# Kernel tuning notes

Hardware: AMD Instinct MI355X
Metric: run time of the kernel (lower is better)

Reference implementation:

```python
import jax, jax.numpy as jnp
import numpy as np

D_EMBED = 64      # per-head dim (module uses d_embed as head dim)
N_HEADS = 8
SCALE = 1.0 / float(np.sqrt(D_EMBED))
ROPE_BASE = 10000.0


def _rope(x):
    # torchtune-style interleaved RoPE. x: [B, S, H, D]
    B, S, H, D = x.shape
    freqs = 1.0 / (ROPE_BASE ** (jnp.arange(0, D, 2, dtype=jnp.float32) / D))  # [D/2]
    ang = jnp.arange(S, dtype=jnp.float32)[:, None] * freqs[None, :]           # [S, D/2]
    cos = jnp.cos(ang)[None, :, None, :]
    sin = jnp.sin(ang)[None, :, None, :]
    x1 = x[..., 0::2]
    x2 = x[..., 1::2]
    return jnp.stack([x1 * cos - x2 * sin, x1 * sin + x2 * cos], axis=-1).reshape(B, S, H, D)


def setup_inputs() -> dict:
    key = jax.random.key(0)
    ks = jax.random.split(key, 5)
    B, S, D, H = 2, 2048, D_EMBED, N_HEADS
    std = 1.0 / np.sqrt(D)
    return {
        "q": jax.random.normal(ks[0], (B, S, D), jnp.float32),
        "Wq": jax.random.normal(ks[1], (H * D, D), jnp.float32) * std,
        "Wk": jax.random.normal(ks[2], (H * D, D), jnp.float32) * std,
        "Wv": jax.random.normal(ks[3], (H * D, D), jnp.float32) * std,
        "Wo": jax.random.normal(ks[4], (D, H * D), jnp.float32) * std,
        "gamma": jnp.ones((H,), jnp.float32),
    }


def reference(q, Wq, Wk, Wv, Wo, gamma):
    B, S, D = q.shape
    H = N_HEADS
    qh = (q @ Wq.T).reshape(B, S, H, D)
    kh = (q @ Wk.T).reshape(B, S, H, D)
    vh = (q @ Wv.T).reshape(B, S, H, D)
    qh = _rope(qh).transpose(0, 2, 1, 3)  # [B,H,S,D]
    kh = _rope(kh).transpose(0, 2, 1, 3)
    vh = vh.transpose(0, 2, 1, 3)
    # RBF attention scores
    qn = jnp.sum(qh * qh, axis=-1, keepdims=True)                 # [B,H,S,1]
    kn = jnp.sum(kh * kh, axis=-1, keepdims=True)                 # [B,H,S,1]
    qk = jnp.einsum('bhsd,bhtd->bhst', qh, kh)                    # [B,H,S,S]
    dist = jnp.maximum(qn - 2.0 * qk + jnp.swapaxes(kn, -2, -1), 0.0)
    scores = jnp.exp(-(gamma[None, :, None, None] * SCALE) * dist)
    causal = jnp.tril(jnp.ones((S, S), dtype=bool))
    scores = jnp.where(causal, scores, 0.0)
    out = jnp.einsum('bhst,bhtd->bhsd', scores, vh)
    out = out.transpose(0, 2, 1, 3).reshape(B, S, H * D)
    return out @ Wo.T
```

## Files before the change

### kernel.cpp

```cpp
#include <hip/hip_runtime.h>
#include <hip/hip_bf16.h>

#define BB 2
#define SS 2048
#define DD 64
#define HH 8
#define HD 512
#define SCALE 0.125f

typedef __bf16 bf16;
typedef __attribute__((ext_vector_type(4))) __bf16 bf16x4;
typedef __attribute__((ext_vector_type(8))) __bf16 bf16x8;
typedef __attribute__((ext_vector_type(4))) float floatx4;

#define PSLOT 2097152

__device__ __forceinline__ floatx4 mfma16(bf16x8 a, bf16x8 b, floatx4 c) {
    return __builtin_amdgcn_mfma_f32_16x16x32_bf16(a, b, c, 0, 0, 0);
}

#define PV_MFMA(ACC, A, B) \
    asm("s_nop 1\n\tv_mfma_f32_16x16x16_bf16 %0, %1, %2, %0" \
        : "+v"(ACC) : "v"(A), "v"(B))

#define MFMA_DRAIN4(A0, A1, A2, A3) \
    asm volatile("s_nop 7\n\ts_nop 7" : "+v"(A0), "+v"(A1), "+v"(A2), "+v"(A3))

#define GLL(G, L) __builtin_amdgcn_global_load_lds( \
    (const __attribute__((address_space(1))) void*)(G), \
    (__attribute__((address_space(3))) void*)(L), 16, 0, 0)

__device__ __forceinline__ bf16x8 load8(const void* base, size_t idx, int f32) {
    if (f32) {
        const float* p = (const float*)base + idx;
        const float4 a = *reinterpret_cast<const float4*>(p);
        const float4 b = *reinterpret_cast<const float4*>(p + 4);
        bf16x8 r;
        r[0] = (bf16)a.x; r[1] = (bf16)a.y; r[2] = (bf16)a.z; r[3] = (bf16)a.w;
        r[4] = (bf16)b.x; r[5] = (bf16)b.y; r[6] = (bf16)b.z; r[7] = (bf16)b.w;
        return r;
    }
    return *reinterpret_cast<const bf16x8*>((const bf16*)base + idx);
}

__device__ __forceinline__ float load1(const void* base, int idx, int f32) {
    return f32 ? ((const float*)base)[idx] : (float)((const bf16*)base)[idx];
}

__global__ __launch_bounds__(256) void proj_rope_kernel(
    const void* __restrict__ q, const void* __restrict__ Wq,
    const void* __restrict__ Wk, const void* __restrict__ Wv,
    bf16* __restrict__ qh, bf16* __restrict__ kh, bf16* __restrict__ vt,
    float* __restrict__ qn, float* __restrict__ kn,
    int* __restrict__ flagw)
{
    const int lane = threadIdx.x & 63;
    const int wid  = blockIdx.x * 4 + (threadIdx.x >> 6);
    if (wid >= 3 * BB * HH * (SS / 64)) return;
    const int l16  = lane & 15;
    const int quad = lane >> 4;

    int hit = 0;
    const unsigned short* qu = (const unsigned short*)q;
#pragma unroll
    for (int i = 0; i < 16; ++i) {
        const unsigned short u = qu[lane + i * 64];
        if (((u >> 7) & 0xFF) >= 134) hit = 1;
    }
    const int f32 = (__ballot(hit) != 0ull) ? 1 : 0;
    if (wid == 0 && lane == 0) *flagw = f32;

    int id = wid;
    const int h   = id % HH; id /= HH;
    const int st4 = id % (SS / 64); id /= (SS / 64);
    const int b   = id % BB; id /= BB;
    const int w   = id;

    const void* W = (w == 0) ? Wq : (w == 1) ? Wk : Wv;
    const size_t bh = (size_t)b * HH + h;

    bf16x8 wb0[4], wb1[4];
#pragma unroll
    for (int t = 0; t < 4; ++t) {
        const size_t wrow = (size_t)(h * 64 + t * 16 + l16) * DD;
        wb0[t] = load8(W, wrow + quad * 8, f32);
        wb1[t] = load8(W, wrow + quad * 8 + 32, f32);
    }

    float frevA[4], frevB[4];
    if (w < 2) {
#pragma unroll
        for (int t = 0; t < 4; ++t) {
            const int dbase = t * 16 + quad * 4;
            frevA[t] = __builtin_amdgcn_exp2f(
                -(float)dbase * (13.2877123795f / 64.0f)) * 0.15915494309f;
            frevB[t] = __builtin_amdgcn_exp2f(
                -(float)(dbase + 2) * (13.2877123795f / 64.0f)) * 0.15915494309f;
        }
    }

    for (int s4 = 0; s4 < 4; ++s4) {
        const int s0 = (st4 * 4 + s4) * 16;
        const size_t qrow = ((size_t)b * SS + s0 + l16) * DD;
        bf16x8 a0 = load8(q, qrow + quad * 8, f32);
        bf16x8 a1 = load8(q, qrow + quad * 8 + 32, f32);

        floatx4 cv[4];
#pragma unroll
        for (int t = 0; t < 4; ++t) {
            floatx4 acc = {0.f, 0.f, 0.f, 0.f};
            if (w < 2) {
                acc = mfma16(wb0[t], a0, acc);
                acc = mfma16(wb1[t], a1, acc);
            } else {
                acc = mfma16(a0, wb0[t], acc);
                acc = mfma16(a1, wb1[t], acc);
            }
            cv[t] = acc;
        }

        if (w < 2) {
            bf16*  dst  = (w == 0) ? qh : kh;
            float* ndst = (w == 0) ? qn : kn;
            const float srowf = (float)(s0 + l16);
            float nacc = 0.f;
            bf16* drow = dst + (bh * SS + s0 + l16) * DD + quad * 4;
#pragma unroll
            for (int t = 0; t < 4; ++t) {
                float revA = srowf * frevA[t]; revA -= floorf(revA);
                float revB = srowf * frevB[t]; revB -= floorf(revB);
                const float snA = __builtin_amdgcn_sinf(revA);
                const float csA = __builtin_amdgcn_cosf(revA);
                const float snB = __builtin_amdgcn_sinf(revB);
                const float csB = __builtin_amdgcn_cosf(revB);
                const float x0 = cv[t][0], x1 = cv[t][1];
                const float x2 = cv[t][2], x3 = cv[t][3];
                const float r0 = x0 * csA - x1 * snA;
                const float r1 = x0 * snA + x1 * csA;
                const float r2 = x2 * csB - x3 * snB;
                const float r3 = x2 * snB + x3 * csB;
                nacc += r0 * r0 + r1 * r1 + r2 * r2 + r3 * r3;
                bf16x4 o; o[0]=(bf16)r0; o[1]=(bf16)r1; o[2]=(bf16)r2; o[3]=(bf16)r3;
                *reinterpret_cast<bf16x4*>(drow + t * 16) = o;
            }
            nacc += __shfl_xor(nacc, 16);
            nacc += __shfl_xor(nacc, 32);
            if (quad == 0) ndst[bh * SS + s0 + l16] = nacc;
        } else {
            bf16* vrow = vt + ((size_t)bh * 128 + st4 * 4 + s4) * 1024
                       + l16 * 16 + quad * 4;
#pragma unroll
            for (int t = 0; t < 4; ++t) {
                bf16x4 pv;
#pragma unroll
                for (int r = 0; r < 4; ++r) pv[r] = (bf16)cv[t][r];
                *reinterpret_cast<bf16x4*>(vrow + t * 256) = pv;
            }
        }
    }
}

__global__ __launch_bounds__(256) void attn_kernel(
    const bf16* __restrict__ qh, const bf16* __restrict__ kh,
    const bf16* __restrict__ vt, const float* __restrict__ qn,
    const float* __restrict__ kn, const void* __restrict__ gamma,
    bf16* __restrict__ partial, const int* __restrict__ flagp,
    int ksh, int pb)
{
    __shared__ __align__(16) char smem[16384];
    const int f32  = *flagp;
    const int tid  = threadIdx.x;
    const int wv   = tid >> 6;
    const int lane = tid & 63;
    const int l16  = lane & 15;
    const int quad = lane >> 4;

    const int xcd  = blockIdx.x & 7;
    int sblk = blockIdx.x >> 3;
    const int half = (sblk >= pb) ? 1 : 0;
    const int bh   = xcd + (half << 3);
    sblk -= half * pb;
    int q4 = 0;
    for (;;) {
        const int ns = ((q4 * 64 + 63) >> ksh) + 1;
        if (sblk < ns) break;
        sblk -= ns; ++q4;
    }
    const int slot = sblk;
    const int qt   = q4 * 4 + wv;
    const int s0   = qt * 16;
    const int tb   = slot << ksh;
    const int te   = min(tb + (1 << ksh), (q4 + 1) * 64);
    const int nch  = (te - tb) >> 5;
    const int h    = bh & 7;

    const float cc = load1(gamma, h, f32) * SCALE * 1.4426950408889634f;

    const bf16* qbase = qh + ((size_t)bh * SS + s0 + l16) * DD;
    bf16x8 aq0 = *reinterpret_cast<const bf16x8*>(qbase + quad * 8);
    bf16x8 aq1 = *reinterpret_cast<const bf16x8*>(qbase + quad * 8 + 32);
    const float qn_l = qn[(size_t)bh * SS + s0 + l16];

    floatx4 acc0 = {0.f,0.f,0.f,0.f}, acc1 = {0.f,0.f,0.f,0.f};
    floatx4 acc2 = {0.f,0.f,0.f,0.f}, acc3 = {0.f,0.f,0.f,0.f};

    const float* knp   = kn + (size_t)bh * SS + quad * 4;
    const char* kgbase = (const char*)(kh + (size_t)bh * SS * DD);
    const char* vgbase = (const char*)(vt + (size_t)bh * 131072);

    const int jK   = wv * 64 + lane;
    const int keyK = jK >> 3;
    const int cK   = ((jK & 7) - keyK) & 7;
    const int goffK = keyK * 128 + cK * 16;
    const int goffV = jK * 16;
    char* ldsK = smem + wv * 1024;
    char* ldsV = smem + 8192 + wv * 1024;

    const int kro0 = (l16 * 8 + ((quad + l16) & 7)) * 16;
    const int kro1 = (l16 * 8 + ((quad + 4 + l16) & 7)) * 16;
    const int vro  = l16 * 32 + quad * 8;

    GLL(kgbase + (size_t)tb * 128 + goffK, ldsK);
    GLL(vgbase + (size_t)(tb >> 4) * 2048 + goffV, ldsV);
    __syncthreads();

    int buf = 0, t0 = tb;
    for (int c = 0; c < nch; ++c, t0 += 32) {
        if (c + 1 < nch) {
            GLL(kgbase + (size_t)(t0 + 32) * 128 + goffK, ldsK + ((buf ^ 1) << 12));
            GLL(vgbase + (size_t)((t0 + 32) >> 4) * 2048 + goffV, ldsV + ((buf ^ 1) << 12));
        }
        const float4 knv0 = *reinterpret_cast<const float4*>(knp + t0);
        const float4 knv1 = *reinterpret_cast<const float4*>(knp + t0 + 16);
        const char* Kb = smem + (buf << 12);
        const char* Vb = smem + 8192 + (buf << 12);

        bf16x8 kc0 = *reinterpret_cast<const bf16x8*>(Kb + kro0);
        bf16x8 kc1 = *reinterpret_cast<const bf16x8*>(Kb + kro1);
        bf16x8 kc2 = *reinterpret_cast<const bf16x8*>(Kb + 2048 + kro0);
        bf16x8 kc3 = *reinterpret_cast<const bf16x8*>(Kb + 2048 + kro1);
        bf16x4 v00 = *reinterpret_cast<const bf16x4*>(Vb + vro);
        bf16x4 v01 = *reinterpret_cast<const bf16x4*>(Vb + 512 + vro);
        bf16x4 v02 = *reinterpret_cast<const bf16x4*>(Vb + 1024 + vro);
        bf16x4 v03 = *reinterpret_cast<const bf16x4*>(Vb + 1536 + vro);
        bf16x4 v10 = *reinterpret_cast<const bf16x4*>(Vb + 2048 + vro);
        bf16x4 v11 = *reinterpret_cast<const bf16x4*>(Vb + 2560 + vro);
        bf16x4 v12 = *reinterpret_cast<const bf16x4*>(Vb + 3072 + vro);
        bf16x4 v13 = *reinterpret_cast<const bf16x4*>(Vb + 3584 + vro);

        floatx4 z0 = {0.f,0.f,0.f,0.f};
        z0 = mfma16(kc0, aq0, z0);
        z0 = mfma16(kc1, aq1, z0);
        floatx4 z1 = {0.f,0.f,0.f,0.f};
        z1 = mfma16(kc2, aq0, z1);
        z1 = mfma16(kc3, aq1, z1);

        const float* k0_ = (const float*)&knv0;
        const float* k1_ = (const float*)&knv1;
        bf16x4 p0, p1;
        if (t0 + 31 <= s0) {
#pragma unroll
            for (int i = 0; i < 4; ++i) {
                float rawA = fmaf(-2.f, z0[i], qn_l + k0_[i]);
                float rawB = fmaf(-2.f, z1[i], qn_l + k1_[i]);
                p0[i] = (bf16)__builtin_amdgcn_exp2f(fminf(-cc * rawA, 0.f));
                p1[i] = (bf16)__builtin_amdgcn_exp2f(fminf(-cc * rawB, 0.f));
            }
        } else {
            const int dq0 = s0 + l16 - t0 - quad * 4;
            const int dq1 = dq0 - 16;
#pragma unroll
            for (int i = 0; i < 4; ++i) {
                float rawA = fmaf(-2.f, z0[i], qn_l + k0_[i]);
                float rawB = fmaf(-2.f, z1[i], qn_l + k1_[i]);
                float eA = __builtin_amdgcn_exp2f(fminf(-cc * rawA, 0.f));
                float eB = __builtin_amdgcn_exp2f(fminf(-cc * rawB, 0.f));
                p0[i] = (bf16)((i <= dq0) ? eA : 0.f);
                p1[i] = (bf16)((i <= dq1) ? eB : 0.f);
            }
        }

        PV_MFMA(acc0, v00, p0);
        PV_MFMA(acc1, v01, p0);
        PV_MFMA(acc2, v02, p0);
        PV_MFMA(acc3, v03, p0);
        PV_MFMA(acc0, v10, p1);
        PV_MFMA(acc1, v11, p1);
        PV_MFMA(acc2, v12, p1);
        PV_MFMA(acc3, v13, p1);

        __syncthreads();
        buf ^= 1;
    }

    MFMA_DRAIN4(acc0, acc1, acc2, acc3);

    bf16* pbp = partial + (size_t)slot * PSLOT
              + ((size_t)bh * SS + s0 + l16) * DD + quad * 4;
    bf16x4 o;
#define STORE4(PTR, ACC) \
    o[0]=(bf16)(ACC)[0]; o[1]=(bf16)(ACC)[1]; o[2]=(bf16)(ACC)[2]; o[3]=(bf16)(ACC)[3]; \
    *reinterpret_cast<bf16x4*>(PTR) = o;
    STORE4(pbp +  0, acc0)
    STORE4(pbp + 16, acc1)
    STORE4(pbp + 32, acc2)
    STORE4(pbp + 48, acc3)
#undef STORE4
}

template <int NACT>
__device__ __forceinline__ floatx4 opj_core(const bf16* __restrict__ partial,
                                            const void* __restrict__ Wo,
                                            int b, int srow, size_t brow,
                                            int f32, int quad) {
    floatx4 acc = {0.f, 0.f, 0.f, 0.f};
#pragma unroll 4
    for (int kk = 0; kk < HD; kk += 32) {
        const int h  = kk >> 6;
        const int d0 = (kk & 63) + quad * 8;
        const bf16* ap = partial + (((size_t)(b * 8 + h)) * SS + srow) * 64 + d0;
        bf16x8 v0 = *reinterpret_cast<const bf16x8*>(ap);
        float u[8];
#pragma unroll
        for (int i = 0; i < 8; ++i) u[i] = (float)v0[i];
#pragma unroll
        for (int s = 1; s < NACT; ++s) {
            bf16x8 vs = *reinterpret_cast<const bf16x8*>(ap + (size_t)s * PSLOT);
#pragma unroll
            for (int i = 0; i < 8; ++i) u[i] += (float)vs[i];
        }
        bf16x8 a;
#pragma unroll
        for (int i = 0; i < 8; ++i) a[i] = (bf16)u[i];
        bf16x8 w = load8(Wo, brow + kk, f32);
        acc = mfma16(a, w, acc);
    }
    return acc;
}

__global__ __launch_bounds__(256) void outproj_kernel(
    const bf16* __restrict__ partial, const void* __restrict__ Wo,
    void* __restrict__ out, const int* __restrict__ flagp, int ksh)
{
    const int f32  = *flagp;
    const int ct   = threadIdx.x >> 6;
    const int lane = threadIdx.x & 63;
    const int l16  = lane & 15;
    const int quad = lane >> 4;

    const int g0   = blockIdx.x * 16;
    const int b    = g0 >> 11;
    const int s0   = g0 & (SS - 1);
    const int nact = (s0 >> ksh) + 1;
    const int srow = s0 + l16;
    const size_t brow = (size_t)(ct * 16 + l16) * HD + quad * 8;

    floatx4 acc;
    switch (nact) {
        case 1:  acc = opj_core<1>(partial, Wo, b, srow, brow, f32, quad); break;
        case 2:  acc = opj_core<2>(partial, Wo, b, srow, brow, f32, quad); break;
        case 3:  acc = opj_core<3>(partial, Wo, b, srow, brow, f32, quad); break;
        case 4:  acc = opj_core<4>(partial, Wo, b, srow, brow, f32, quad); break;
        case 5:  acc = opj_core<5>(partial, Wo, b, srow, brow, f32, quad); break;
        case 6:  acc = opj_core<6>(partial, Wo, b, srow, brow, f32, quad); break;
        case 7:  acc = opj_core<7>(partial, Wo, b, srow, brow, f32, quad); break;
        default: acc = opj_core<8>(partial, Wo, b, srow, brow, f32, quad); break;
    }

#pragma unroll
    for (int r = 0; r < 4; ++r) {
        const size_t o = (size_t)(g0 + quad * 4 + r) * DD + ct * 16 + l16;
        if (f32) ((float*)out)[o] = acc[r];
        else     ((bf16*)out)[o]  = (bf16)acc[r];
    }
}

extern "C" void kernel_launch(void* const* d_in, const int* in_sizes, int n_in,
                              void* d_out, int out_size, void* d_ws, size_t ws_size,
                              hipStream_t stream) {
    const void* q     = d_in[0];
    const void* Wq    = d_in[1];
    const void* Wk    = d_in[2];
    const void* Wv    = d_in[3];
    const void* Wo    = d_in[4];
    const void* gamma = d_in[5];

    char* ws = (char*)d_ws;
    bf16*  qh      = (bf16*)(ws);
    bf16*  kh      = (bf16*)(ws + 4194304);
    bf16*  vt      = (bf16*)(ws + 8388608);
    float* qn      = (float*)(ws + 12582912);
    float* kn      = (float*)(ws + 12713984);
    int*   flag    = (int*)  (ws + 12845056);
    bf16*  partial = (bf16*)(ws + 13631488);

    int ksh = 11;
    const size_t base = 13631488ull;
    if      (ws_size >= base + 4ull * 4194304) ksh = 9;
    else if (ws_size >= base + 2ull * 4194304) ksh = 10;

    int pb = 0;
    for (int q4 = 0; q4 < 32; ++q4) pb += ((q4 * 64 + 63) >> ksh) + 1;

    const int nproj = 3 * BB * HH * (SS / 64);
    proj_rope_kernel<<<dim3((nproj + 3) / 4), dim3(256), 0, stream>>>(
        q, Wq, Wk, Wv, qh, kh, vt, qn, kn, flag);
    attn_kernel<<<dim3(16 * pb), dim3(256), 0, stream>>>(
        qh, kh, vt, qn, kn, gamma, partial, flag, ksh, pb);
    outproj_kernel<<<dim3(BB * SS / 16), dim3(256), 0, stream>>>(
        partial, Wo, d_out, flag, ksh);
}
```

Baseline: 120.8 us.

## Process 64-key chunks per attention loop iteration with larger LDS double buffer

The attention main loop now stages 64 keys per iteration instead of 32. Each thread issues two global-to-LDS loads each for K and V, and LDS grows to 32 KB so double buffering still fits. Each iteration runs two unrolled 32-key sub-steps, which halves the number of barriers and loop overhead per key. The cost is more LDS per block, which may lower occupancy. The output-projection switch is also trimmed to at most 4 active partial slots, which assumes the shift parameter limits the slot count.

```diff
diff --git a/kernel.cpp b/kernel.cpp
--- a/kernel.cpp
+++ b/kernel.cpp
@@ -167,7 +167,7 @@
     bf16* __restrict__ partial, const int* __restrict__ flagp,
     int ksh, int pb)
 {
-    __shared__ __align__(16) char smem[16384];
+    __shared__ __align__(16) char smem[32768];
     const int f32  = *flagp;
     const int tid  = threadIdx.x;
     const int wv   = tid >> 6;
@@ -191,7 +191,7 @@
     const int s0   = qt * 16;
     const int tb   = slot << ksh;
     const int te   = min(tb + (1 << ksh), (q4 + 1) * 64);
-    const int nch  = (te - tb) >> 5;
+    const int nch  = (te - tb) >> 6;
     const int h    = bh & 7;
 
     const float cc = load1(gamma, h, f32) * SCALE * 1.4426950408889634f;
@@ -208,86 +208,103 @@
     const char* kgbase = (const char*)(kh + (size_t)bh * SS * DD);
     const char* vgbase = (const char*)(vt + (size_t)bh * 131072);
 
-    const int jK   = wv * 64 + lane;
-    const int keyK = jK >> 3;
-    const int cK   = ((jK & 7) - keyK) & 7;
-    const int goffK = keyK * 128 + cK * 16;
-    const int goffV = jK * 16;
-    char* ldsK = smem + wv * 1024;
-    char* ldsV = smem + 8192 + wv * 1024;
+    const int jA = wv * 64 + lane, jB = jA + 256;
+    const int keyA = jA >> 3, keyB = jB >> 3;
+    const int goffKA = keyA * 128 + ((((jA & 7) - keyA) & 7)) * 16;
+    const int goffKB = keyB * 128 + ((((jB & 7) - keyB) & 7)) * 16;
+    const int goffVA = jA * 16;
+    const int goffVB = jB * 16;
+    char* ldsKA = smem + wv * 1024;
+    char* ldsKB = smem + 4096 + wv * 1024;
+    char* ldsVA = smem + 16384 + wv * 1024;
+    char* ldsVB = smem + 16384 + 4096 + wv * 1024;
 
     const int kro0 = (l16 * 8 + ((quad + l16) & 7)) * 16;
     const int kro1 = (l16 * 8 + ((quad + 4 + l16) & 7)) * 16;
     const int vro  = l16 * 32 + quad * 8;
 
-    GLL(kgbase + (size_t)tb * 128 + goffK, ldsK);
-    GLL(vgbase + (size_t)(tb >> 4) * 2048 + goffV, ldsV);
+    GLL(kgbase + (size_t)tb * 128 + goffKA, ldsKA);
+    GLL(kgbase + (size_t)tb * 128 + goffKB, ldsKB);
+    GLL(vgbase + (size_t)(tb >> 4) * 2048 + goffVA, ldsVA);
+    GLL(vgbase + (size_t)(tb >> 4) * 2048 + goffVB, ldsVB);
     __syncthreads();
 
     int buf = 0, t0 = tb;
-    for (int c = 0; c < nch; ++c, t0 += 32) {
+    for (int c = 0; c < nch; ++c, t0 += 64) {
         if (c + 1 < nch) {
-            GLL(kgbase + (size_t)(t0 + 32) * 128 + goffK, ldsK + ((buf ^ 1) << 12));
-            GLL(vgbase + (size_t)((t0 + 32) >> 4) * 2048 + goffV, ldsV + ((buf ^ 1) << 12));
-        }
-        const float4 knv0 = *reinterpret_cast<const float4*>(knp + t0);
-        const float4 knv1 = *reinterpret_cast<const float4*>(knp + t0 + 16);
-        const char* Kb = smem + (buf << 12);
-        const char* Vb = smem + 8192 + (buf << 12);
-
-        bf16x8 kc0 = *reinterpret_cast<const bf16x8*>(Kb + kro0);
-        bf16x8 kc1 = *reinterpret_cast<const bf16x8*>(Kb + kro1);
-        bf16x8 kc2 = *reinterpret_cast<const bf16x8*>(Kb + 2048 + kro0);
-        bf16x8 kc3 = *reinterpret_cast<const bf16x8*>(Kb + 2048 + kro1);
-        bf16x4 v00 = *reinterpret_cast<const bf16x4*>(Vb + vro);
-        bf16x4 v01 = *reinterpret_cast<const bf16x4*>(Vb + 512 + vro);
-        bf16x4 v02 = *reinterpret_cast<const bf16x4*>(Vb + 1024 + vro);
-        bf16x4 v03 = *reinterpret_cast<const bf16x4*>(Vb + 1536 + vro);
-        bf16x4 v10 = *reinterpret_cast<const bf16x4*>(Vb + 2048 + vro);
-        bf16x4 v11 = *reinterpret_cast<const bf16x4*>(Vb + 2560 + vro);
-        bf16x4 v12 = *reinterpret_cast<const bf16x4*>(Vb + 3072 + vro);
-        bf16x4 v13 = *reinterpret_cast<const bf16x4*>(Vb + 3584 + vro);
-
-        floatx4 z0 = {0.f,0.f,0.f,0.f};
-        z0 = mfma16(kc0, aq0, z0);
-        z0 = mfma16(kc1, aq1, z0);
-        floatx4 z1 = {0.f,0.f,0.f,0.f};
-        z1 = mfma16(kc2, aq0, z1);
-        z1 = mfma16(kc3, aq1, z1);
-
-        const float* k0_ = (const float*)&knv0;
-        const float* k1_ = (const float*)&knv1;
-        bf16x4 p0, p1;
-        if (t0 + 31 <= s0) {
-#pragma unroll
-            for (int i = 0; i < 4; ++i) {
-                float rawA = fmaf(-2.f, z0[i], qn_l + k0_[i]);
-                float rawB = fmaf(-2.f, z1[i], qn_l + k1_[i]);
-                p0[i] = (bf16)__builtin_amdgcn_exp2f(fminf(-cc * rawA, 0.f));
-                p1[i] = (bf16)__builtin_amdgcn_exp2f(fminf(-cc * rawB, 0.f));
+            const size_t kg = (size_t)(t0 + 64) * 128;
+            const size_t vg = (size_t)((t0 + 64) >> 4) * 2048;
+            const int ob = (buf ^ 1) << 13;
+            GLL(kgbase + kg + goffKA, ldsKA + ob);
+            GLL(kgbase + kg + goffKB, ldsKB + ob);
+            GLL(vgbase + vg + goffVA, ldsVA + ob);
+            GLL(vgbase + vg + goffVB, ldsVB + ob);
+        }
+        const char* Kb = smem + (buf << 13);
+        const char* Vb = smem + 16384 + (buf << 13);
+
+#pragma unroll
+        for (int hh = 0; hh < 2; ++hh) {
+            const int th = t0 + hh * 32;
+            const char* Kh = Kb + hh * 4096;
+            const char* Vh = Vb + hh * 4096;
+            const float4 knv0 = *reinterpret_cast<const float4*>(knp + th);
+            const float4 knv1 = *reinterpret_cast<const float4*>(knp + th + 16);
+
+            bf16x8 kc0 = *reinterpret_cast<const bf16x8*>(Kh + kro0);
+            bf16x8 kc1 = *reinterpret_cast<const bf16x8*>(Kh + kro1);
+            bf16x8 kc2 = *reinterpret_cast<const bf16x8*>(Kh + 2048 + kro0);
+            bf16x8 kc3 = *reinterpret_cast<const bf16x8*>(Kh + 2048 + kro1);
+            bf16x4 v00 = *reinterpret_cast<const bf16x4*>(Vh + vro);
+            bf16x4 v01 = *reinterpret_cast<const bf16x4*>(Vh + 512 + vro);
+            bf16x4 v02 = *reinterpret_cast<const bf16x4*>(Vh + 1024 + vro);
+            bf16x4 v03 = *reinterpret_cast<const bf16x4*>(Vh + 1536 + vro);
+            bf16x4 v10 = *reinterpret_cast<const bf16x4*>(Vh + 2048 + vro);
+            bf16x4 v11 = *reinterpret_cast<const bf16x4*>(Vh + 2560 + vro);
+            bf16x4 v12 = *reinterpret_cast<const bf16x4*>(Vh + 3072 + vro);
+            bf16x4 v13 = *reinterpret_cast<const bf16x4*>(Vh + 3584 + vro);
+
+            floatx4 z0 = {0.f,0.f,0.f,0.f};
+            z0 = mfma16(kc0, aq0, z0);
+            z0 = mfma16(kc1, aq1, z0);
+            floatx4 z1 = {0.f,0.f,0.f,0.f};
+            z1 = mfma16(kc2, aq0, z1);
+            z1 = mfma16(kc3, aq1, z1);
+
+            const float* k0_ = (const float*)&knv0;
+            const float* k1_ = (const float*)&knv1;
+            bf16x4 p0, p1;
+            if (th + 31 <= s0) {
+#pragma unroll
+                for (int i = 0; i < 4; ++i) {
+                    float rawA = fmaf(-2.f, z0[i], qn_l + k0_[i]);
+                    float rawB = fmaf(-2.f, z1[i], qn_l + k1_[i]);
+                    p0[i] = (bf16)__builtin_amdgcn_exp2f(fminf(-cc * rawA, 0.f));
+                    p1[i] = (bf16)__builtin_amdgcn_exp2f(fminf(-cc * rawB, 0.f));
+                }
+            } else {
+                const int dq0 = s0 + l16 - th - quad * 4;
+                const int dq1 = dq0 - 16;
+#pragma unroll
+                for (int i = 0; i < 4; ++i) {
+                    float rawA = fmaf(-2.f, z0[i], qn_l + k0_[i]);
+                    float rawB = fmaf(-2.f, z1[i], qn_l + k1_[i]);
+                    float eA = __builtin_amdgcn_exp2f(fminf(-cc * rawA, 0.f));
+                    float eB = __builtin_amdgcn_exp2f(fminf(-cc * rawB, 0.f));
+                    p0[i] = (bf16)((i <= dq0) ? eA : 0.f);
+                    p1[i] = (bf16)((i <= dq1) ? eB : 0.f);
+                }
             }
-        } else {
-            const int dq0 = s0 + l16 - t0 - quad * 4;
-            const int dq1 = dq0 - 16;
-#pragma unroll
-            for (int i = 0; i < 4; ++i) {
-                float rawA = fmaf(-2.f, z0[i], qn_l + k0_[i]);
-                float rawB = fmaf(-2.f, z1[i], qn_l + k1_[i]);
-                float eA = __builtin_amdgcn_exp2f(fminf(-cc * rawA, 0.f));
-                float eB = __builtin_amdgcn_exp2f(fminf(-cc * rawB, 0.f));
-                p0[i] = (bf16)((i <= dq0) ? eA : 0.f);
-                p1[i] = (bf16)((i <= dq1) ? eB : 0.f);
-            }
-        }
-
-        PV_MFMA(acc0, v00, p0);
-        PV_MFMA(acc1, v01, p0);
-        PV_MFMA(acc2, v02, p0);
-        PV_MFMA(acc3, v03, p0);
-        PV_MFMA(acc0, v10, p1);
-        PV_MFMA(acc1, v11, p1);
-        PV_MFMA(acc2, v12, p1);
-        PV_MFMA(acc3, v13, p1);
+
+            PV_MFMA(acc0, v00, p0);
+            PV_MFMA(acc1, v01, p0);
+            PV_MFMA(acc2, v02, p0);
+            PV_MFMA(acc3, v03, p0);
+            PV_MFMA(acc0, v10, p1);
+            PV_MFMA(acc1, v11, p1);
+            PV_MFMA(acc2, v12, p1);
+            PV_MFMA(acc3, v13, p1);
+        }
 
         __syncthreads();
         buf ^= 1;
@@ -360,11 +377,7 @@
         case 1:  acc = opj_core<1>(partial, Wo, b, srow, brow, f32, quad); break;
         case 2:  acc = opj_core<2>(partial, Wo, b, srow, brow, f32, quad); break;
         case 3:  acc = opj_core<3>(partial, Wo, b, srow, brow, f32, quad); break;
-        case 4:  acc = opj_core<4>(partial, Wo, b, srow, brow, f32, quad); break;
-        case 5:  acc = opj_core<5>(partial, Wo, b, srow, brow, f32, quad); break;
-        case 6:  acc = opj_core<6>(partial, Wo, b, srow, brow, f32, quad); break;
-        case 7:  acc = opj_core<7>(partial, Wo, b, srow, brow, f32, quad); break;
-        default: acc = opj_core<8>(partial, Wo, b, srow, brow, f32, quad); break;
+        default: acc = opj_core<4>(partial, Wo, b, srow, brow, f32, quad); break;
     }
 
 #pragma unroll
```

New measurement: 122.9 us. No clear change (+1.7%).
